# Kernel tuning notes

Hardware: AMD Instinct MI355X
Metric: run time of the kernel (lower is better)

Reference implementation:

```python
import jax, jax.numpy as jnp
import numpy as np

WINDOW_SIZE = 9
EPS = 1e-05


def _box_sum(x, w):
    """Zero-padded 3D box-filter sum, computed separably (one 1D conv per axis).
    Identical math to conv3d with an all-ones [w,w,w] kernel and zero padding."""
    pad = w // 2
    dn = ('NCDHW', 'OIDHW', 'NCDHW')
    for ax in range(3):  # D, H, W
        kshape = [1, 1, 1, 1, 1]
        kshape[2 + ax] = w
        kernel = jnp.ones(kshape, x.dtype)
        padding = [(0, 0)] * 3
        padding[ax] = (pad, pad)
        x = jax.lax.conv_general_dilated(x, kernel, (1, 1, 1), padding,
                                         dimension_numbers=dn)
    return x


def setup_inputs() -> dict:
    key = jax.random.key(0)
    k1, k2 = jax.random.split(key)
    shape = (2, 1, 160, 160, 160)
    predicted = jax.random.uniform(k1, shape, dtype=jnp.float32)
    target = jax.random.uniform(k2, shape, dtype=jnp.float32)
    return {"predicted": predicted, "target": target}


def reference(predicted, target):
    I = predicted.astype(jnp.float32)
    J = target.astype(jnp.float32)
    w = WINDOW_SIZE
    win_size = jnp.float32(w ** 3)

    I_sum = _box_sum(I, w)
    J_sum = _box_sum(J, w)
    I2_sum = _box_sum(I * I, w)
    J2_sum = _box_sum(J * J, w)
    IJ_sum = _box_sum(I * J, w)

    u_I = I_sum / win_size
    u_J = J_sum / win_size

    cross = IJ_sum - u_J * I_sum - u_I * J_sum + u_I * u_J * win_size
    I_var = I2_sum - 2.0 * u_I * I_sum + u_I * u_I * win_size
    J_var = J2_sum - 2.0 * u_J * J_sum + u_J * u_J * win_size

    cc = cross * cross / (I_var * J_var + EPS)
    cc = jnp.clip(cc, 0.0, 1.0)
    return 1.0 - jnp.mean(cc)
```

## Files before the change

### kernel.cpp

```cpp
#include <hip/hip_runtime.h>
#include <hip/hip_fp16.h>


#define DIM 160
#define HW  (160 * 160)
#define VOL (160 * 160 * 160)
#define NBATCH 2
#define TH 8
#define SR 16
#define THB 320
#define SEG 10
#define NSEG (DIM / SEG)
#define NK2BLK 800

struct __align__(16) h8 { __half2 a, b, c, d; };
struct __align__(8) h4 { __half2 a, b; };
typedef float v2f __attribute__((ext_vector_type(2)));

__device__ inline float4 dec8(unsigned int u) {
    v2f lo = __builtin_amdgcn_cvt_pk_f32_fp8((int)u, false);
    v2f hi = __builtin_amdgcn_cvt_pk_f32_fp8((int)u, true);
    return make_float4(lo[0], lo[1], hi[0], hi[1]);
}

__device__ inline unsigned int enc8(float a, float b, float c, float d) {
    int u = __builtin_amdgcn_cvt_pk_fp8_f32(a, b, 0, false);
    u = __builtin_amdgcn_cvt_pk_fp8_f32(c, d, u, true);
    return (unsigned int)u;
}

__global__ __launch_bounds__(THB) void k1_boxsum2d(const float* __restrict__ I,
                                                   const float* __restrict__ J,
                                                   unsigned char* __restrict__ A8) {
    __shared__ __half wsl[5][SR][DIM];

    const int tid = threadIdx.x;
    const int orig = blockIdx.x;
    const int wgid = (orig & 7) * 800 + (orig >> 3);
    const int ty = wgid % 20;
    const int rest = wgid / 20;
    const int d = rest % DIM;
    const int batch = rest / DIM;
    const int h0 = ty * TH;
    const float* Ib = I + (size_t)batch * VOL + (size_t)d * HW;
    const float* Jb = J + (size_t)batch * VOL + (size_t)d * HW;

    {
        const int r = tid / 20, g = tid % 20;
        const int gh = h0 - 4 + r;
        const int gw = 8 * g - 4;
        __half* wrow = &wsl[0][0][0] + (r * DIM + 8 * g);

        if (gh < 0 || gh >= DIM) {
            const __half2 hz = __float2half2_rn(0.f);
            h8 z; z.a = hz; z.b = hz; z.c = hz; z.d = hz;
#pragma unroll
            for (int ch = 0; ch < 5; ++ch)
                *(h8*)(wrow + ch * (SR * DIM)) = z;
        } else {
            const float* pI = Ib + gh * DIM;
            const float* pJ = Jb + gh * DIM;
            float a[16], b[16];
#pragma unroll
            for (int q = 0; q < 4; ++q) {
                int c0 = gw + 4 * q;
                if (c0 >= 0 && c0 < DIM) {
                    *(float4*)&a[4 * q] = *(const float4*)(pI + c0);
                    *(float4*)&b[4 * q] = *(const float4*)(pJ + c0);
                } else {
                    *(float4*)&a[4 * q] = make_float4(0.f, 0.f, 0.f, 0.f);
                    *(float4*)&b[4 * q] = make_float4(0.f, 0.f, 0.f, 0.f);
                }
            }
#define PROC(CH, VAL)                                                       \
            {                                                               \
                float o[8];                                                 \
                float ss = 0.f;                                             \
                _Pragma("unroll")                                           \
                for (int k = 0; k < 9; ++k) { ss += (VAL); }                \
                o[0] = ss;                                                  \
                _Pragma("unroll")                                           \
                for (int j = 1; j < 8; ++j) {                               \
                    int k = j + 8; float add_ = (VAL);                      \
                    k = j - 1;     float sub_ = (VAL);                      \
                    ss += add_ - sub_;                                      \
                    o[j] = ss;                                              \
                }                                                           \
                h8 v;                                                       \
                v.a = __floats2half2_rn(o[0], o[1]);                        \
                v.b = __floats2half2_rn(o[2], o[3]);                        \
                v.c = __floats2half2_rn(o[4], o[5]);                        \
                v.d = __floats2half2_rn(o[6], o[7]);                        \
                *(h8*)(wrow + CH * (SR * DIM)) = v;                         \
            }
            PROC(0, a[k])
            PROC(1, b[k])
            PROC(2, a[k] * a[k])
            PROC(3, b[k] * b[k])
            PROC(4, a[k] * b[k])
#undef PROC
        }
    }
    __syncthreads();

    {
        const int q = tid % 40, r8 = tid / 40;
        const int wp0 = 2 * q;
        const size_t ob = (size_t)batch * 5 * VOL + (size_t)d * HW +
                          (size_t)(h0 + r8) * DIM + 4 * q;
#pragma unroll
        for (int ch = 0; ch < 5; ++ch) {
            const __half2* col = (const __half2*)&wsl[ch][r8][0] + wp0;
            h4 v = *(const h4*)col;
            __half2 sa = v.a, sb = v.b;
#pragma unroll
            for (int k = 1; k < 9; ++k) {
                h4 u = *(const h4*)(col + k * (DIM / 2));
                sa = __hadd2(sa, u.a);
                sb = __hadd2(sb, u.b);
            }
            float2 f0 = __half22float2(sa);
            float2 f1 = __half22float2(sb);
            *(unsigned int*)(A8 + ob + (size_t)ch * VOL) =
                enc8(f0.x, f0.y, f1.x, f1.y);
        }
    }
}

__device__ inline void cc_accum(float s0, float s1, float s2, float s3,
                                float s4, float& acc) {
    const float inv_wsz = 1.0f / 729.0f;
    float cross = s4 - s0 * s1 * inv_wsz;
    float Ivar  = s2 - s0 * s0 * inv_wsz;
    float Jvar  = s3 - s1 * s1 * inv_wsz;
    float cc = cross * cross * __builtin_amdgcn_rcpf(Ivar * Jvar + 1e-5f);
    acc += fminf(fmaxf(cc, 0.0f), 1.0f);
}

__global__ __launch_bounds__(256) void k2_dsum_final(const unsigned char* __restrict__ A8,
                                                     float* __restrict__ partial) {
    const int batch = blockIdx.y;
    const unsigned int* B = (const unsigned int*)(A8 + (size_t)batch * 5 * VOL);
    const int PLW = VOL / 4;
    const int HWW = HW / 4;
    int t = blockIdx.x * 256 + threadIdx.x;
    int wq = t % 40;
    int rest = t / 40;
    int h = rest % DIM;
    int seg = rest / DIM;
    int d0 = seg * SEG;
    const int base = h * 40 + wq;

    float4 s0 = {0,0,0,0}, s1 = {0,0,0,0}, s2 = {0,0,0,0},
           s3 = {0,0,0,0}, s4 = {0,0,0,0};
#define ACC4(sv, ch, idx, sgn)                                              \
    {                                                                       \
        float4 v_ = dec8(B[(ch) * PLW + (idx)]);                            \
        sv.x sgn v_.x; sv.y sgn v_.y; sv.z sgn v_.z; sv.w sgn v_.w;         \
    }
#pragma unroll
    for (int k = -4; k <= 4; ++k) {
        int dd = d0 + k;
        if (dd >= 0) {
            int idx = base + dd * HWW;
            ACC4(s0, 0, idx, +=) ACC4(s1, 1, idx, +=) ACC4(s2, 2, idx, +=)
            ACC4(s3, 3, idx, +=) ACC4(s4, 4, idx, +=)
        }
    }

    float acc = 0.f;
    for (int d = d0; d < d0 + SEG; ++d) {
        cc_accum(s0.x, s1.x, s2.x, s3.x, s4.x, acc);
        cc_accum(s0.y, s1.y, s2.y, s3.y, s4.y, acc);
        cc_accum(s0.z, s1.z, s2.z, s3.z, s4.z, acc);
        cc_accum(s0.w, s1.w, s2.w, s3.w, s4.w, acc);
        int lead = d + 5, trail = d - 4;
        if (lead < DIM) {
            int li = base + lead * HWW;
            ACC4(s0, 0, li, +=) ACC4(s1, 1, li, +=) ACC4(s2, 2, li, +=)
            ACC4(s3, 3, li, +=) ACC4(s4, 4, li, +=)
        }
        if (trail >= 0) {
            int ti = base + trail * HWW;
            ACC4(s0, 0, ti, -=) ACC4(s1, 1, ti, -=) ACC4(s2, 2, ti, -=)
            ACC4(s3, 3, ti, -=) ACC4(s4, 4, ti, -=)
        }
    }
#undef ACC4

#pragma unroll
    for (int off = 32; off > 0; off >>= 1) acc += __shfl_down(acc, off);
    __shared__ float ws4[4];
    if ((threadIdx.x & 63) == 0) ws4[threadIdx.x >> 6] = acc;
    __syncthreads();
    if (threadIdx.x == 0)
        partial[batch * 400 + blockIdx.x] = ws4[0] + ws4[1] + ws4[2] + ws4[3];
}

__global__ __launch_bounds__(256) void final_reduce(const float* __restrict__ partial,
                                                    int n, float* __restrict__ out) {
    float a = 0.f;
    for (int i = threadIdx.x; i < n; i += 256) a += partial[i];
#pragma unroll
    for (int off = 32; off > 0; off >>= 1) a += __shfl_down(a, off);
    __shared__ float ws4[4];
    if ((threadIdx.x & 63) == 0) ws4[threadIdx.x >> 6] = a;
    __syncthreads();
    if (threadIdx.x == 0)
        out[0] = 1.0f - (ws4[0] + ws4[1] + ws4[2] + ws4[3]) *
                            (1.0f / (float)(NBATCH * VOL));
}

extern "C" void kernel_launch(void* const* d_in, const int* in_sizes, int n_in,
                              void* d_out, int out_size, void* d_ws, size_t ws_size,
                              hipStream_t stream) {
    const float* I = (const float*)d_in[0];
    const float* J = (const float*)d_in[1];
    float* out = (float*)d_out;

    unsigned char* A8 = (unsigned char*)d_ws;
    float* partial = (float*)(A8 + (size_t)NBATCH * 5 * VOL);

    k1_boxsum2d<<<20 * DIM * NBATCH, THB, 0, stream>>>(I, J, A8);
    dim3 g2(400, NBATCH);
    k2_dsum_final<<<g2, 256, 0, stream>>>(A8, partial);
    final_reduce<<<1, 256, 0, stream>>>(partial, NK2BLK, out);
}
```

Before: 53.93 us.

## Tile k1 box-sum along W into 32-wide tiles with 64-thread blocks

Splits each k1 block's work, previously a full 160-wide row strip of 8 output rows, into five 32-wide column tiles, each handled by a single 64-thread wavefront using a smaller padded shared-memory tile. This gives five times as many small blocks, which improves scheduling granularity and lowers LDS use per block. In exchange, the 4-column halo on each side is reloaded and recomputed for every tile, so global reads rise from 160 to 200 columns per 160 outputs. Each block also runs only one wave.

After: 60.12 us. 1.11x slower.

```diff
diff --git a/kernel.cpp b/kernel.cpp
--- a/kernel.cpp
+++ b/kernel.cpp
@@ -7,8 +7,8 @@
 #define VOL (160 * 160 * 160)
 #define NBATCH 2
 #define TH 8
-#define SR 16
-#define THB 320
+#define TW 32
+#define SRP 40
 #define SEG 10
 #define NSEG (DIM / SEG)
 #define NK2BLK 800
@@ -29,34 +29,36 @@
     return (unsigned int)u;
 }
 
-__global__ __launch_bounds__(THB) void k1_boxsum2d(const float* __restrict__ I,
-                                                   const float* __restrict__ J,
-                                                   unsigned char* __restrict__ A8) {
-    __shared__ __half wsl[5][SR][DIM];
+__global__ __launch_bounds__(64) void k1_boxsum2d(const float* __restrict__ I,
+                                                  const float* __restrict__ J,
+                                                  unsigned char* __restrict__ A8) {
+    __shared__ __half wsl[5][16][SRP];
 
     const int tid = threadIdx.x;
     const int orig = blockIdx.x;
-    const int wgid = (orig & 7) * 800 + (orig >> 3);
-    const int ty = wgid % 20;
-    const int rest = wgid / 20;
+    const int wgid = (orig & 7) * 4000 + (orig >> 3);
+    const int tx = wgid % 5;
+    int rest = wgid / 5;
+    const int ty = rest % 20;
+    rest /= 20;
     const int d = rest % DIM;
     const int batch = rest / DIM;
-    const int h0 = ty * TH;
+    const int h0 = ty * TH, w0 = tx * TW;
     const float* Ib = I + (size_t)batch * VOL + (size_t)d * HW;
     const float* Jb = J + (size_t)batch * VOL + (size_t)d * HW;
 
     {
-        const int r = tid / 20, g = tid % 20;
+        const int r = tid >> 2, g = tid & 3;
         const int gh = h0 - 4 + r;
-        const int gw = 8 * g - 4;
-        __half* wrow = &wsl[0][0][0] + (r * DIM + 8 * g);
+        const int gw = w0 + 8 * g - 4;
+        __half* wrow = &wsl[0][r][8 * g];
 
         if (gh < 0 || gh >= DIM) {
             const __half2 hz = __float2half2_rn(0.f);
             h8 z; z.a = hz; z.b = hz; z.c = hz; z.d = hz;
 #pragma unroll
             for (int ch = 0; ch < 5; ++ch)
-                *(h8*)(wrow + ch * (SR * DIM)) = z;
+                *(h8*)(wrow + ch * (16 * SRP)) = z;
         } else {
             const float* pI = Ib + gh * DIM;
             const float* pJ = Jb + gh * DIM;
@@ -91,7 +93,7 @@
                 v.b = __floats2half2_rn(o[2], o[3]);                        \
                 v.c = __floats2half2_rn(o[4], o[5]);                        \
                 v.d = __floats2half2_rn(o[6], o[7]);                        \
-                *(h8*)(wrow + CH * (SR * DIM)) = v;                         \
+                *(h8*)(wrow + CH * (16 * SRP)) = v;                         \
             }
             PROC(0, a[k])
             PROC(1, b[k])
@@ -104,18 +106,17 @@
     __syncthreads();
 
     {
-        const int q = tid % 40, r8 = tid / 40;
-        const int wp0 = 2 * q;
+        const int q = tid & 7, r8 = tid >> 3;
         const size_t ob = (size_t)batch * 5 * VOL + (size_t)d * HW +
-                          (size_t)(h0 + r8) * DIM + 4 * q;
+                          (size_t)(h0 + r8) * DIM + w0 + 4 * q;
 #pragma unroll
         for (int ch = 0; ch < 5; ++ch) {
-            const __half2* col = (const __half2*)&wsl[ch][r8][0] + wp0;
+            const __half2* col = (const __half2*)&wsl[ch][r8][0] + 2 * q;
             h4 v = *(const h4*)col;
             __half2 sa = v.a, sb = v.b;
 #pragma unroll
             for (int k = 1; k < 9; ++k) {
-                h4 u = *(const h4*)(col + k * (DIM / 2));
+                h4 u = *(const h4*)(col + k * (SRP / 2));
                 sa = __hadd2(sa, u.a);
                 sb = __hadd2(sb, u.b);
             }
@@ -221,7 +222,7 @@
     unsigned char* A8 = (unsigned char*)d_ws;
     float* partial = (float*)(A8 + (size_t)NBATCH * 5 * VOL);
 
-    k1_boxsum2d<<<20 * DIM * NBATCH, THB, 0, stream>>>(I, J, A8);
+    k1_boxsum2d<<<20 * 5 * DIM * NBATCH, 64, 0, stream>>>(I, J, A8);
     dim3 g2(400, NBATCH);
     k2_dsum_final<<<g2, 256, 0, stream>>>(A8, partial);
     final_reduce<<<1, 256, 0, stream>>>(partial, NK2BLK, out);
```
